# Kernel optimization log

Hardware: AMD Instinct MI355X
Metric: run time of the kernel (lower is better)

Reference implementation:

```python
import jax, jax.numpy as jnp
import numpy as np

K = 16  # kNN size (self included)
R = 4   # upsampling ratio


def _knn(pts, k):
    # pts: (B,N,3) -> idx (B,N,k); smallest distance first, so idx[:,:,0] is self
    sq = jnp.sum(pts * pts, axis=-1)
    d = sq[:, :, None] - 2.0 * jnp.einsum('bnd,bmd->bnm', pts, pts) + sq[:, None, :]
    _, idx = jax.lax.top_k(-d, k)
    return idx


def _gather(feats, idx):
    # feats (B,N,C), idx (B,N,k) -> (B,N,k,C)
    return jax.vmap(lambda f, i: f[i])(feats, idx)


def _conv1d(x, w, b):  # pointwise Conv1d: x (B,C,N)
    return jnp.einsum('oc,bcn->bon', w, x) + b[None, :, None]


def _conv2d(x, w, b):  # pointwise Conv2d: x (B,C,N,K)
    return jnp.einsum('oc,bcnk->bonk', w, x) + b[None, :, None, None]


def setup_inputs() -> dict:
    key = jax.random.key(0)
    ks = jax.random.split(key, 16)
    B, N = 2, 8192
    w = lambda k, s: jax.random.normal(k, s, jnp.float32) * 0.1
    return {
        'x': jax.random.normal(ks[0], (B, 3, N), jnp.float32),
        'mlp1_w1': w(ks[1], (32, 3)), 'mlp1_b1': jnp.zeros((32,), jnp.float32),
        'mlp1_w2': w(ks[2], (64, 32)), 'mlp1_b2': jnp.zeros((64,), jnp.float32),
        'mlp2_w1': w(ks[3], (32, 9)), 'mlp2_b1': jnp.zeros((32,), jnp.float32),
        'mlp3_w1': w(ks[4], (128, 96)), 'mlp3_b1': jnp.zeros((128,), jnp.float32),
        'mlp3_w2': w(ks[5], (12, 128)), 'mlp3_b2': jnp.zeros((12,), jnp.float32),
        'att_w1': w(ks[6], (128, 64)), 'att_b1': jnp.zeros((128,), jnp.float32),
        'att_w2': w(ks[7], (64, 128)), 'att_b2': jnp.zeros((64,), jnp.float32),
    }


def reference(x, mlp1_w1, mlp1_b1, mlp1_w2, mlp1_b2, mlp2_w1, mlp2_b1,
              mlp3_w1, mlp3_b1, mlp3_w2, mlp3_b2,
              att_w1, att_b1, att_w2, att_b2):
    B, C, N = x.shape
    pts = jnp.transpose(x, (0, 2, 1))                     # (B,N,3)
    idx = _knn(jax.lax.stop_gradient(pts), K)             # (B,N,K)

    # local 3x3 covariance features -> (B,9,N)
    nb = _gather(pts, idx)                                # (B,N,K,3)
    c = nb - jnp.mean(nb, axis=2, keepdims=True)
    cov = jnp.einsum('bnki,bnkj->bnij', c, c) / K         # (B,N,3,3)
    cov_feat = jnp.transpose(cov.reshape(B, N, 9), (0, 2, 1))

    # mlp1: 3 -> 32 -> 64, relu on both (last_act=True)
    f1 = jax.nn.relu(_conv1d(jax.nn.relu(_conv1d(x, mlp1_w1, mlp1_b1)), mlp1_w2, mlp1_b2))

    # gather neighbor features (exclude self) and form relative features
    fk = _gather(jnp.transpose(f1, (0, 2, 1)), idx[:, :, 1:])   # (B,N,K-1,64)
    f_knn = jnp.transpose(fk, (0, 3, 1, 2)) - f1[:, :, :, None]  # (B,64,N,K-1)

    # attention MLP (2D): 64 -> 128 -> 64, softmax over neighbor axis
    h = jax.nn.relu(_conv2d(f_knn, att_w1, att_b1))
    w = jax.nn.softmax(_conv2d(h, att_w2, att_b2), axis=-1)
    f_agg = jnp.sum(w * f_knn, axis=-1)                   # (B,64,N)

    # mlp2: 9 -> 32 with relu
    f_cov = jax.nn.relu(_conv1d(cov_feat, mlp2_w1, mlp2_b1))     # (B,32,N)

    f = jnp.concatenate([f_agg, f_cov], axis=1)           # (B,96,N)
    g = _conv1d(jax.nn.relu(_conv1d(f, mlp3_w1, mlp3_b1)), mlp3_w2, mlp3_b2)  # (B,3R,N)

    return jnp.tile(x, (1, 1, R)) + 0.15 * g.reshape(B, -1, R * N)
```

## Files before the change

kernel.cpp:

```cpp
#include <hip/hip_runtime.h>

#define BB 2
#define NN 8192
#define KK 16
#define QPB 64
#define PRE 256
#define STASH 32
#define EPSF 0.02f
typedef unsigned long long ull;
typedef unsigned short ushort;
#define KINF 0xFFFFFFFFFFFFFFFFULL
#define BFONE 0x3F80

typedef __attribute__((ext_vector_type(8))) short short8;
typedef __attribute__((ext_vector_type(4))) float f32x4;

static __device__ __forceinline__ ushort f2bf(float f) {
    unsigned u = __float_as_uint(f);
    unsigned r = (u + 0x7FFFu + ((u >> 16) & 1u)) >> 16;
    return (ushort)r;
}
static __device__ __forceinline__ float bf2f(ushort s) {
    return __uint_as_float(((unsigned)s) << 16);
}

static __device__ __forceinline__ float distq(const float4& qp, const float4& cn) {
    return fmaf(qp.x, cn.x, fmaf(qp.y, cn.y, fmaf(qp.z, cn.z, __fadd_rn(qp.w, cn.w))));
}

__global__ __launch_bounds__(256) void prep_f1_kernel(
    const float* __restrict__ x, float4* __restrict__ pts4, float4* __restrict__ pts4n,
    ushort* __restrict__ ptsC64,
    const float* __restrict__ w1, const float* __restrict__ b1,
    const float* __restrict__ w2, const float* __restrict__ b2,
    ushort* __restrict__ f1)
{
    if (blockIdx.x < 64) {
        int t = blockIdx.x * 256 + threadIdx.x;
        int b = t >> 13, n = t & (NN - 1);
        float x0 = x[(b * 3 + 0) * NN + n];
        float x1 = x[(b * 3 + 1) * NN + n];
        float x2 = x[(b * 3 + 2) * NN + n];
        float sq = fmaf(x2, x2, fmaf(x1, x1, __fmul_rn(x0, x0)));
        pts4[t]  = make_float4(x0, x1, x2, sq);
        pts4n[t] = make_float4(-2.f * x0, -2.f * x1, -2.f * x2, sq);

        float m2x = -2.f * x0, m2y = -2.f * x1, m2z = -2.f * x2;
        ushort hx = f2bf(m2x), hy = f2bf(m2y), hz = f2bf(m2z);
        ushort lx = f2bf(m2x - bf2f(hx));
        ushort ly = f2bf(m2y - bf2f(hy));
        ushort lz = f2bf(m2z - bf2f(hz));
        ushort sh = f2bf(sq), sl = f2bf(sq - bf2f(sh));
        short8 r0 = { (short)hx, (short)hy, (short)hz, (short)lx,
                      (short)ly, (short)lz, (short)hx, (short)hy };
        short8 r1 = { (short)hz, (short)lx, (short)ly, (short)lz,
                      (short)sh, (short)sl, (short)BFONE, (short)BFONE };
        short8 zz = { 0, 0, 0, 0, 0, 0, 0, 0 };
        ushort* cp = ptsC64 + (size_t)t * 32;
        *(short8*)(cp)      = r0;
        *(short8*)(cp + 8)  = r1;
        *(short8*)(cp + 16) = zz;
        *(short8*)(cp + 24) = zz;
    } else {
        int P = (blockIdx.x - 64) * 256 + threadIdx.x;
        int b = P >> 13, n = P & (NN - 1);
        float x0 = x[(b * 3 + 0) * NN + n];
        float x1 = x[(b * 3 + 1) * NN + n];
        float x2 = x[(b * 3 + 2) * NN + n];
        float h[32];
#pragma unroll
        for (int o = 0; o < 32; ++o) {
            float v = fmaf(w1[o * 3 + 2], x2, fmaf(w1[o * 3 + 1], x1, fmaf(w1[o * 3 + 0], x0, b1[o])));
            h[o] = fmaxf(v, 0.f);
        }
#pragma unroll
        for (int o4 = 0; o4 < 16; ++o4) {
            float vv[4];
#pragma unroll
            for (int u = 0; u < 4; ++u) {
                int o = o4 * 4 + u;
                float v = b2[o];
#pragma unroll
                for (int k = 0; k < 32; ++k) v = fmaf(w2[o * 32 + k], h[k], v);
                vv[u] = fmaxf(v, 0.f);
            }
            ushort4 s = { f2bf(vv[0]), f2bf(vv[1]), f2bf(vv[2]), f2bf(vv[3]) };
            *(ushort4*)(f1 + (size_t)P * 64 + o4 * 4) = s;
        }
    }
}

__global__ __launch_bounds__(512) void knn_prefix_kernel(
    const float4* __restrict__ pts4, const float4* __restrict__ pts4n,
    float* __restrict__ thrb)
{
    __shared__ float pbuf[11 * 512];
    __shared__ float smem[8 * 4 * 64];

    const int t    = threadIdx.x;
    const int wv   = t >> 6;
    const int lane = t & 63;
    const int b    = blockIdx.y;
    const int q    = blockIdx.x * QPB + lane;
    const int sl   = __builtin_amdgcn_readfirstlane(wv);

    const float4 qp = pts4[b * NN + q];
    const float4* __restrict__ cp = pts4n + (size_t)b * NN + (size_t)sl * 1024;

    float l0 = 3.0e38f, l1 = 3.0e38f, l2 = 3.0e38f, l3 = 3.0e38f;
    float curmax = 3.0e38f;
    int pend = 0;

    for (int i0 = 0; i0 < PRE; i0 += 8) {
#pragma unroll
        for (int u = 0; u < 8; ++u) {
            float d = distq(qp, cp[i0 + u]);
            pbuf[pend * 512 + t] = d;
            pend += (d < curmax) ? 1 : 0;
        }
        if (__any(pend >= 4)) {
            for (int j = 0; j < 11; ++j) {
                if (!__any(j < pend)) break;
                float v = pbuf[j * 512 + t];
                float k = (j < pend) ? v : 3.0e38f;
                bool b3 = k < l3, b2 = k < l2, b1 = k < l1, b0 = k < l0;
                l3 = b3 ? (b2 ? l2 : k) : l3;
                l2 = b2 ? (b1 ? l1 : k) : l2;
                l1 = b1 ? (b0 ? l0 : k) : l1;
                l0 = b0 ? k : l0;
            }
            pend = 0;
            curmax = l3;
        }
    }
    for (int j = 0; j < 11; ++j) {
        if (!__any(j < pend)) break;
        float v = pbuf[j * 512 + t];
        float k = (j < pend) ? v : 3.0e38f;
        bool b3 = k < l3, b2 = k < l2, b1 = k < l1, b0 = k < l0;
        l3 = b3 ? (b2 ? l2 : k) : l3;
        l2 = b2 ? (b1 ? l1 : k) : l2;
        l1 = b1 ? (b0 ? l0 : k) : l1;
        l0 = b0 ? k : l0;
    }

    __syncthreads();
    smem[(wv * 4 + 0) * 64 + lane] = l0;
    smem[(wv * 4 + 1) * 64 + lane] = l1;
    smem[(wv * 4 + 2) * 64 + lane] = l2;
    smem[(wv * 4 + 3) * 64 + lane] = l3;
    __syncthreads();

    if (t < QPB) {
        float h[8];
        int kc[8];
#pragma unroll
        for (int s = 0; s < 8; ++s) { h[s] = smem[(s * 4) * 64 + t]; kc[s] = 0; }
        float best = 3.0e38f;
        for (int o = 0; o < KK; ++o) {
            best = h[0]; int bs = 0;
#pragma unroll
            for (int s = 1; s < 8; ++s) { if (h[s] < best) { best = h[s]; bs = s; } }
#pragma unroll
            for (int s = 0; s < 8; ++s) {
                if (s == bs) {
                    kc[s]++;
                    h[s] = (kc[s] < 4) ? smem[(s * 4 + kc[s]) * 64 + t] : 3.0e38f;
                }
            }
        }
        thrb[(size_t)b * NN + blockIdx.x * QPB + t] = best;
    }
}

__global__ __launch_bounds__(256) void knn_scan_kernel(
    const float4* __restrict__ pts4, const ushort* __restrict__ ptsC64,
    const float* __restrict__ thrb, unsigned* __restrict__ bufm)
{
    __shared__ __align__(16) char lbuf[10240];

    const int t    = threadIdx.x;
    const int wv   = t >> 6;
    const int lane = t & 63;
    const int l15  = lane & 15, l4 = lane >> 4;
    const int b    = blockIdx.y;
    const int z    = blockIdx.z;
    const int qt   = blockIdx.x * 4 + wv;
    const int qbase = qt * 16;

    const float4 p = pts4[(size_t)b * NN + qbase + l15];
    const ushort qhx = f2bf(p.x), qhy = f2bf(p.y), qhz = f2bf(p.z);
    const ushort qlx = f2bf(p.x - bf2f(qhx));
    const ushort qly = f2bf(p.y - bf2f(qhy));
    const ushort qlz = f2bf(p.z - bf2f(qhz));
    const ushort qsh = f2bf(p.w), qsl = f2bf(p.w - bf2f(qsh));
    short8 qf;
    if (l4 == 0)
        qf = short8{ (short)qhx, (short)qhy, (short)qhz, (short)qhx,
                     (short)qhy, (short)qhz, (short)qlx, (short)qly };
    else if (l4 == 1)
        qf = short8{ (short)qlz, (short)qlx, (short)qly, (short)qlz,
                     (short)BFONE, (short)BFONE, (short)qsh, (short)qsl };
    else
        qf = short8{ 0, 0, 0, 0, 0, 0, 0, 0 };

    const float thrq = thrb[(size_t)b * NN + qbase + l15] * 1.001f + EPSF;

    const uint4* __restrict__ gsrc =
        (const uint4*)(ptsC64 + ((size_t)b * NN + (size_t)z * 1024) * 32);

    unsigned* __restrict__ op =
        bufm + (size_t)(b * NN + qbase + l15) * 256 + z * 32 + l4 * 8;

    uint4 r0 = gsrc[t], r1 = gsrc[t + 256];
    unsigned w4[4];

#pragma unroll 1
    for (int g = 0; g < 8; ++g) {
        __syncthreads();
        *(uint4*)(lbuf + (t >> 2) * 80 + (t & 3) * 16) = r0;
        *(uint4*)(lbuf + ((t + 256) >> 2) * 80 + (t & 3) * 16) = r1;
        if (g < 7) {
            r0 = gsrc[(g + 1) * 512 + t];
            r1 = gsrc[(g + 1) * 512 + t + 256];
        }
        __syncthreads();

        unsigned acc = 0;
#pragma unroll
        for (int i = 0; i < 8; ++i) {
            short8 cf = *(const short8*)(lbuf + (i * 16 + l15) * 80 + l4 * 16);
            f32x4 D = { 0.f, 0.f, 0.f, 0.f };
            D = __builtin_amdgcn_mfma_f32_16x16x32_bf16(cf, qf, D, 0, 0, 0);
            acc = acc * 2u + (unsigned)(D[0] <= thrq);
            acc = acc * 2u + (unsigned)(D[1] <= thrq);
            acc = acc * 2u + (unsigned)(D[2] <= thrq);
            acc = acc * 2u + (unsigned)(D[3] <= thrq);
        }
        w4[g & 3] = acc;
        if ((g & 3) == 3)
            *(uint4*)(op + (g >> 2) * 4) = make_uint4(w4[0], w4[1], w4[2], w4[3]);
    }
}

__global__ __launch_bounds__(256) void knn_select_kernel(
    const float4* __restrict__ pts4, const float4* __restrict__ pts4n,
    const unsigned* __restrict__ bufm,
    int* __restrict__ iout)
{
    __shared__ ull sm3[4][8][8][KK];
    __shared__ ushort stash[STASH][256];

    const int t = threadIdx.x;
    const int wv = t >> 6, lane = t & 63;
    const int qq = lane & 7, hh = lane >> 3;
    const int q  = (blockIdx.x * 4 + wv) * 8 + qq;
    const int b  = q >> 13;

    const float4 qp = pts4[q];
    ull list[KK];
#pragma unroll
    for (int i = 0; i < KK; ++i) list[i] = KINF;

    const unsigned* __restrict__ mrow = bufm + (size_t)q * 256 + hh * 32;
    int pend = 0;
#pragma unroll 1
    for (int g4 = 0; g4 < 8; ++g4) {
        uint4 v = ((const uint4*)mrow)[g4];
        unsigned wsv[4] = { v.x, v.y, v.z, v.w };
#pragma unroll
        for (int j = 0; j < 4; ++j) {
            unsigned w = wsv[j];
            const int W = hh * 32 + g4 * 4 + j;
            const int cb = ((W >> 5) << 10) + ((W & 7) << 7) + (((W >> 3) & 3) << 2);
            while (w) {
                int p = __builtin_ctz(w);
                w &= w - 1;
                int m = 31 - p;
                int id = cb + ((m >> 2) << 4) + (m & 3);
                if (pend < STASH) {
                    stash[pend][t] = (ushort)id;
                    ++pend;
                } else {
                    float d = distq(qp, pts4n[b * NN + id]);
                    unsigned ud = __float_as_uint(d);
                    ud ^= ((unsigned)((int)ud >> 31)) | 0x80000000u;
                    ull k = ((ull)ud << 32) | (unsigned)id;
#pragma unroll
                    for (int i2 = KK - 1; i2 > 0; --i2) {
                        bool c1 = k < list[i2];
                        bool c2 = k < list[i2 - 1];
                        ull nd = c2 ? list[i2 - 1] : k;
                        list[i2] = c1 ? nd : list[i2];
                    }
                    list[0] = (k < list[0]) ? k : list[0];
                }
            }
        }
    }

    for (int j = 0; ; j += 2) {
        if (!__any(j < pend)) break;
        int j1 = j + 1;
        int id0 = stash[(j  < pend) ? j  : 0][t];
        int id1 = stash[(j1 < pend) ? j1 : 0][t];
        float4 cn0 = pts4n[b * NN + id0];
        float4 cn1 = pts4n[b * NN + id1];

        float d0 = distq(qp, cn0);
        unsigned ud0 = __float_as_uint(d0);
        ud0 ^= ((unsigned)((int)ud0 >> 31)) | 0x80000000u;
        ull k0 = (j < pend) ? ((((ull)ud0) << 32) | (unsigned)id0) : KINF;
#pragma unroll
        for (int i2 = KK - 1; i2 > 0; --i2) {
            bool c1 = k0 < list[i2];
            bool c2 = k0 < list[i2 - 1];
            ull nd = c2 ? list[i2 - 1] : k0;
            list[i2] = c1 ? nd : list[i2];
        }
        list[0] = (k0 < list[0]) ? k0 : list[0];

        float d1 = distq(qp, cn1);
        unsigned ud1 = __float_as_uint(d1);
        ud1 ^= ((unsigned)((int)ud1 >> 31)) | 0x80000000u;
        ull k1 = (j1 < pend) ? ((((ull)ud1) << 32) | (unsigned)id1) : KINF;
#pragma unroll
        for (int i2 = KK - 1; i2 > 0; --i2) {
            bool c1 = k1 < list[i2];
            bool c2 = k1 < list[i2 - 1];
            ull nd = c2 ? list[i2 - 1] : k1;
            list[i2] = c1 ? nd : list[i2];
        }
        list[0] = (k1 < list[0]) ? k1 : list[0];
    }

#pragma unroll
    for (int k = 0; k < KK; ++k) sm3[wv][hh][qq][k] = list[k];

    if (hh == 0) {
        ull h[8]; int kc[8];
#pragma unroll
        for (int s = 0; s < 8; ++s) { h[s] = sm3[wv][s][qq][0]; kc[s] = 0; }
        int* op = iout + (size_t)q * KK;
        for (int o = 0; o < KK; ++o) {
            ull best = h[0]; int bs = 0;
#pragma unroll
            for (int s = 1; s < 8; ++s) { if (h[s] < best) { best = h[s]; bs = s; } }
            op[o] = (int)(unsigned)(best & 0xFFFFFFFFULL);
#pragma unroll
            for (int s = 0; s < 8; ++s) {
                if (s == bs) {
                    kc[s]++;
                    h[s] = (kc[s] < KK) ? sm3[wv][s][qq][kc[s]] : KINF;
                }
            }
        }
    }
}

__global__ __launch_bounds__(256, 2) void attn_cov_kernel(
    const ushort* __restrict__ f1, const int* __restrict__ idx,
    const float* __restrict__ aw1, const float* __restrict__ ab1,
    const float* __restrict__ aw2, const float* __restrict__ ab2,
    ushort* __restrict__ fagg,
    const float4* __restrict__ pts4,
    const float* __restrict__ cw, const float* __restrict__ cb,
    ushort* __restrict__ fcov)
{
    __shared__ __align__(16) ushort w1l[128][72];
    __shared__ __align__(16) ushort w2l[64][136];
    __shared__ __align__(16) ushort fkb[4][16][72];
    __shared__ __align__(16) ushort hb[4][16][136];

    const int t = threadIdx.x;

    if (blockIdx.x >= 512) {
        int P = (blockIdx.x - 512) * 256 + t;
        int b = P >> 13;
        const int4* ip4 = (const int4*)(idx + (size_t)P * KK);
        int ids[KK];
#pragma unroll
        for (int g = 0; g < 4; ++g) {
            int4 v = ip4[g];
            ids[g * 4 + 0] = v.x; ids[g * 4 + 1] = v.y;
            ids[g * 4 + 2] = v.z; ids[g * 4 + 3] = v.w;
        }
        float px[KK], py[KK], pz[KK];
#pragma unroll
        for (int k = 0; k < KK; ++k) {
            float4 c = pts4[b * NN + ids[k]];
            px[k] = c.x; py[k] = c.y; pz[k] = c.z;
        }
        float mx = 0.f, my = 0.f, mz = 0.f;
#pragma unroll
        for (int k = 0; k < KK; ++k) { mx += px[k]; my += py[k]; mz += pz[k]; }
        mx *= (1.f / 16.f); my *= (1.f / 16.f); mz *= (1.f / 16.f);
        float c00 = 0, c01 = 0, c02 = 0, c11 = 0, c12 = 0, c22 = 0;
#pragma unroll
        for (int k = 0; k < KK; ++k) {
            float dx = px[k] - mx, dy = py[k] - my, dz = pz[k] - mz;
            c00 = fmaf(dx, dx, c00); c01 = fmaf(dx, dy, c01); c02 = fmaf(dx, dz, c02);
            c11 = fmaf(dy, dy, c11); c12 = fmaf(dy, dz, c12); c22 = fmaf(dz, dz, c22);
        }
        const float inv = 1.f / 16.f;
        float cf[9] = { c00 * inv, c01 * inv, c02 * inv,
                        c01 * inv, c11 * inv, c12 * inv,
                        c02 * inv, c12 * inv, c22 * inv };
        ushort* outp = fcov + (size_t)P * 32;
#pragma unroll
        for (int o = 0; o < 32; ++o) {
            float v = cb[o];
#pragma unroll
            for (int m = 0; m < 9; ++m) v = fmaf(cw[o * 9 + m], cf[m], v);
            outp[o] = f2bf(fmaxf(v, 0.f));
        }
        return;
    }

    const int wv = t >> 6, lane = t & 63;
    const int l15 = lane & 15, qd = lane >> 4;

    for (int i = t; i < 128 * 64; i += 256) {
        int r = i >> 6, c = i & 63;
        w1l[r][c] = f2bf(aw1[i]);
    }
    for (int i = t; i < 64 * 128; i += 256) {
        int r = i >> 7, c = i & 127;
        w2l[r][c] = f2bf(aw2[i]);
    }
    __syncthreads();

    const int W = blockIdx.x * 4 + wv;
    for (int g = 0; g < 8; ++g) {
        const int P = W * 8 + g;
        const int b = P >> 13;

        float fc = bf2f(f1[(size_t)P * 64 + lane]);
        ushort fn[15];
#pragma unroll
        for (int j = 0; j < 15; ++j) {
            int nb = idx[(size_t)P * KK + 1 + j];
            fn[j] = f1[((size_t)b * NN + nb) * 64 + lane];
        }
#pragma unroll
        for (int j = 0; j < 15; ++j) fkb[wv][j][lane] = f2bf(bf2f(fn[j]) - fc);
        fkb[wv][15][lane] = 0;

        short8 a0 = *(const short8*)&fkb[wv][l15][qd * 8];
        short8 a1 = *(const short8*)&fkb[wv][l15][32 + qd * 8];

#pragma unroll
        for (int tile = 0; tile < 8; ++tile) {
            float bv = ab1[tile * 16 + l15];
            f32x4 acc = { bv, bv, bv, bv };
            short8 b0 = *(const short8*)&w1l[tile * 16 + l15][qd * 8];
            short8 b1f = *(const short8*)&w1l[tile * 16 + l15][32 + qd * 8];
            acc = __builtin_amdgcn_mfma_f32_16x16x32_bf16(a0, b0, acc, 0, 0, 0);
            acc = __builtin_amdgcn_mfma_f32_16x16x32_bf16(a1, b1f, acc, 0, 0, 0);
#pragma unroll
            for (int reg = 0; reg < 4; ++reg)
                hb[wv][qd * 4 + reg][tile * 16 + l15] = f2bf(fmaxf(acc[reg], 0.f));
        }

        short8 a2[4];
#pragma unroll
        for (int ks = 0; ks < 4; ++ks)
            a2[ks] = *(const short8*)&hb[wv][l15][ks * 32 + qd * 8];

        f32x4 L[4];
#pragma unroll
        for (int tile = 0; tile < 4; ++tile) {
            float bv = ab2[tile * 16 + l15];
            f32x4 acc = { bv, bv, bv, bv };
#pragma unroll
            for (int ks = 0; ks < 4; ++ks) {
                short8 bf = *(const short8*)&w2l[tile * 16 + l15][ks * 32 + qd * 8];
                acc = __builtin_amdgcn_mfma_f32_16x16x32_bf16(a2[ks], bf, acc, 0, 0, 0);
            }
            L[tile] = acc;
        }

        float fa[4];
#pragma unroll
        for (int tile = 0; tile < 4; ++tile) {
            float m1 = -3.0e38f;
#pragma unroll
            for (int reg = 0; reg < 4; ++reg)
                if (qd * 4 + reg < 15) m1 = fmaxf(m1, L[tile][reg]);
            m1 = fmaxf(m1, __shfl_xor(m1, 16));
            m1 = fmaxf(m1, __shfl_xor(m1, 32));
            float e[4], ssum = 0.f;
#pragma unroll
            for (int reg = 0; reg < 4; ++reg) {
                bool valid = (qd * 4 + reg < 15);
                e[reg] = valid ? __expf(L[tile][reg] - m1) : 0.f;
                ssum += e[reg];
            }
            ssum += __shfl_xor(ssum, 16);
            ssum += __shfl_xor(ssum, 32);
            float part = 0.f;
#pragma unroll
            for (int reg = 0; reg < 4; ++reg) {
                float fkv = bf2f(fkb[wv][qd * 4 + reg][tile * 16 + l15]);
                part = fmaf(e[reg], fkv, part);
            }
            part += __shfl_xor(part, 16);
            part += __shfl_xor(part, 32);
            fa[tile] = part / ssum;
        }
        if (qd == 0) {
#pragma unroll
            for (int tile = 0; tile < 4; ++tile)
                fagg[(size_t)P * 64 + tile * 16 + l15] = f2bf(fa[tile]);
        }
    }
}

__global__ __launch_bounds__(256) void mlp3_kernel(
    const ushort* __restrict__ fagg, const ushort* __restrict__ fcov,
    const float* __restrict__ w1, const float* __restrict__ b1,
    const float* __restrict__ w2, const float* __restrict__ b2,
    const float* __restrict__ x, float* __restrict__ out)
{
    __shared__ __align__(16) ushort fb[4][16][104];
    __shared__ __align__(16) ushort hb[4][16][136];

    const int t = threadIdx.x;
    const int wv = t >> 6, lane = t & 63;
    const int l15 = lane & 15, qd = lane >> 4;

    short8 w1f[8][3];
#pragma unroll
    for (int tile = 0; tile < 8; ++tile)
#pragma unroll
        for (int ks = 0; ks < 3; ++ks) {
            const float* p = w1 + ((size_t)(tile * 16 + l15) * 96 + ks * 32 + qd * 8);
            float4 A = *(const float4*)p, B = *(const float4*)(p + 4);
            short8 f;
            f[0] = f2bf(A.x); f[1] = f2bf(A.y); f[2] = f2bf(A.z); f[3] = f2bf(A.w);
            f[4] = f2bf(B.x); f[5] = f2bf(B.y); f[6] = f2bf(B.z); f[7] = f2bf(B.w);
            w1f[tile][ks] = f;
        }
    short8 w2f[4];
#pragma unroll
    for (int ks = 0; ks < 4; ++ks) {
        short8 f = {};
        if (l15 < 12) {
            const float* p = w2 + ((size_t)l15 * 128 + ks * 32 + qd * 8);
            float4 A = *(const float4*)p, B = *(const float4*)(p + 4);
            f[0] = f2bf(A.x); f[1] = f2bf(A.y); f[2] = f2bf(A.z); f[3] = f2bf(A.w);
            f[4] = f2bf(B.x); f[5] = f2bf(B.y); f[6] = f2bf(B.z); f[7] = f2bf(B.w);
        }
        w2f[ks] = f;
    }

    const int T = blockIdx.x * 4 + wv;

    {
        const int pt = lane >> 2, c4 = lane & 3;
        const ushort* fap = fagg + ((size_t)(T * 16 + pt) * 64 + c4 * 16);
        *(short8*)&fb[wv][pt][c4 * 16]     = *(const short8*)(fap);
        *(short8*)&fb[wv][pt][c4 * 16 + 8] = *(const short8*)(fap + 8);
        const ushort* fcp = fcov + ((size_t)(T * 16 + pt) * 32 + c4 * 8);
        *(short8*)&fb[wv][pt][64 + c4 * 8] = *(const short8*)(fcp);
    }

    short8 a[3];
#pragma unroll
    for (int ks = 0; ks < 3; ++ks)
        a[ks] = *(const short8*)&fb[wv][l15][ks * 32 + qd * 8];

#pragma unroll
    for (int tile = 0; tile < 8; ++tile) {
        float bv = b1[tile * 16 + l15];
        f32x4 acc = { bv, bv, bv, bv };
#pragma unroll
        for (int ks = 0; ks < 3; ++ks)
            acc = __builtin_amdgcn_mfma_f32_16x16x32_bf16(a[ks], w1f[tile][ks], acc, 0, 0, 0);
#pragma unroll
        for (int reg = 0; reg < 4; ++reg)
            hb[wv][qd * 4 + reg][tile * 16 + l15] = f2bf(fmaxf(acc[reg], 0.f));
    }

    short8 a2[4];
#pragma unroll
    for (int ks = 0; ks < 4; ++ks)
        a2[ks] = *(const short8*)&hb[wv][l15][ks * 32 + qd * 8];

    float bv2 = (l15 < 12) ? b2[l15] : 0.f;
    f32x4 acc = { bv2, bv2, bv2, bv2 };
#pragma unroll
    for (int ks = 0; ks < 4; ++ks)
        acc = __builtin_amdgcn_mfma_f32_16x16x32_bf16(a2[ks], w2f[ks], acc, 0, 0, 0);

    if (l15 < 12) {
        const int c = l15 >> 2, rr = l15 & 3;
#pragma unroll
        for (int reg = 0; reg < 4; ++reg) {
            int P = T * 16 + qd * 4 + reg;
            int b = P >> 13, n = P & (NN - 1);
            float xv = x[((size_t)b * 3 + c) * NN + n];
            out[(((size_t)b * 3 + c) * 4 + rr) * NN + n] = xv + 0.15f * acc[reg];
        }
    }
}

extern "C" void kernel_launch(void* const* d_in, const int* in_sizes, int n_in,
                              void* d_out, int out_size, void* d_ws, size_t ws_size,
                              hipStream_t stream)
{
    (void)in_sizes; (void)n_in; (void)out_size; (void)ws_size;
    const float* x    = (const float*)d_in[0];
    const float* m1w1 = (const float*)d_in[1];
    const float* m1b1 = (const float*)d_in[2];
    const float* m1w2 = (const float*)d_in[3];
    const float* m1b2 = (const float*)d_in[4];
    const float* m2w1 = (const float*)d_in[5];
    const float* m2b1 = (const float*)d_in[6];
    const float* m3w1 = (const float*)d_in[7];
    const float* m3b1 = (const float*)d_in[8];
    const float* m3w2 = (const float*)d_in[9];
    const float* m3b2 = (const float*)d_in[10];
    const float* aw1  = (const float*)d_in[11];
    const float* ab1  = (const float*)d_in[12];
    const float* aw2  = (const float*)d_in[13];
    const float* ab2  = (const float*)d_in[14];
    float* out = (float*)d_out;

    char* ws = (char*)d_ws;
    float4* pts4   = (float4*)(ws + 0);
    float4* pts4n  = (float4*)(ws + 262144);
    float*  thrb   = (float*)(ws + 524288);
    int*    idxb   = (int*)  (ws + 589824);
    ushort* ptsC64 = (ushort*)(ws + 1638400);
    unsigned* bufm = (unsigned*)(ws + 2686976);
    ushort* f1b    = (ushort*)(ws + 19464192);
    ushort* fagg   = (ushort*)(ws + 21561344);
    ushort* fcov   = (ushort*)(ws + 23658496);

    prep_f1_kernel<<<128, 256, 0, stream>>>(x, pts4, pts4n, ptsC64, m1w1, m1b1, m1w2, m1b2, f1b);
    knn_prefix_kernel<<<dim3(NN / QPB, BB), 512, 0, stream>>>(pts4, pts4n, thrb);
    knn_scan_kernel<<<dim3(128, BB, 8), 256, 0, stream>>>(pts4, ptsC64, thrb, bufm);
    knn_select_kernel<<<512, 256, 0, stream>>>(pts4, pts4n, bufm, idxb);
    attn_cov_kernel<<<576, 256, 0, stream>>>(f1b, idxb, aw1, ab1, aw2, ab2, fagg,
                                             pts4, m2w1, m2b1, fcov);
    mlp3_kernel<<<256, 256, 0, stream>>>(fagg, fcov, m3w1, m3b1, m3w2, m3b2, x, out);
}
```

Measured before the change: 253.7 us.

## Split kNN prefix threshold across 16 waves with double-buffered candidate loads

The prefix kernel that estimates a per-query kNN distance threshold now runs 1024 threads (16 waves) instead of 512. Each wave scans a 128-point prefix of a 512-point slice, down from 256 points of a 1024-point slice. Candidate loads are double-buffered in registers so the next 8 points are fetched while the current 8 are processed. The final merge covers 16 per-wave top-4 lists instead of 8. Total prefix samples stay at 2048 per query, but the threshold may differ, which can change how many candidates the later scan keeps. The larger block also uses more shared memory.

```diff
diff --git a/kernel.cpp b/kernel.cpp
--- a/kernel.cpp
+++ b/kernel.cpp
@@ -4,7 +4,8 @@
 #define NN 8192
 #define KK 16
 #define QPB 64
-#define PRE 256
+#define PRE2 128
+#define SLICE 512
 #define STASH 32
 #define EPSF 0.02f
 typedef unsigned long long ull;
@@ -90,12 +91,26 @@
     }
 }
 
-__global__ __launch_bounds__(512) void knn_prefix_kernel(
+#define DRAIN_TOP4()                                             \
+    {                                                            \
+        for (int j = 0; j < 11; ++j) {                           \
+            if (!__any(j < pend)) break;                         \
+            float v = pbuf[j * 1024 + t];                        \
+            float k = (j < pend) ? v : 3.0e38f;                  \
+            bool b3 = k < l3, b2 = k < l2, b1 = k < l1, b0 = k < l0; \
+            l3 = b3 ? (b2 ? l2 : k) : l3;                        \
+            l2 = b2 ? (b1 ? l1 : k) : l2;                        \
+            l1 = b1 ? (b0 ? l0 : k) : l1;                        \
+            l0 = b0 ? k : l0;                                    \
+        }                                                        \
+    }
+
+__global__ __launch_bounds__(1024, 4) void knn_prefix_kernel(
     const float4* __restrict__ pts4, const float4* __restrict__ pts4n,
     float* __restrict__ thrb)
 {
-    __shared__ float pbuf[11 * 512];
-    __shared__ float smem[8 * 4 * 64];
+    __shared__ float pbuf[11 * 1024];
+    __shared__ float smem[16 * 4 * 64];
 
     const int t    = threadIdx.x;
     const int wv   = t >> 6;
@@ -105,44 +120,40 @@
     const int sl   = __builtin_amdgcn_readfirstlane(wv);
 
     const float4 qp = pts4[b * NN + q];
-    const float4* __restrict__ cp = pts4n + (size_t)b * NN + (size_t)sl * 1024;
+    const float4* __restrict__ cp = pts4n + (size_t)b * NN + (size_t)sl * SLICE;
 
     float l0 = 3.0e38f, l1 = 3.0e38f, l2 = 3.0e38f, l3 = 3.0e38f;
     float curmax = 3.0e38f;
     int pend = 0;
 
-    for (int i0 = 0; i0 < PRE; i0 += 8) {
+    float4 ca[8], cb2[8];
+#pragma unroll
+    for (int u = 0; u < 8; ++u) ca[u] = cp[u];
+
+#pragma unroll 1
+    for (int i0 = 0; i0 < PRE2; i0 += 16) {
+#pragma unroll
+        for (int u = 0; u < 8; ++u) cb2[u] = cp[i0 + 8 + u];
 #pragma unroll
         for (int u = 0; u < 8; ++u) {
-            float d = distq(qp, cp[i0 + u]);
-            pbuf[pend * 512 + t] = d;
+            float d = distq(qp, ca[u]);
+            pbuf[pend * 1024 + t] = d;
             pend += (d < curmax) ? 1 : 0;
         }
-        if (__any(pend >= 4)) {
-            for (int j = 0; j < 11; ++j) {
-                if (!__any(j < pend)) break;
-                float v = pbuf[j * 512 + t];
-                float k = (j < pend) ? v : 3.0e38f;
-                bool b3 = k < l3, b2 = k < l2, b1 = k < l1, b0 = k < l0;
-                l3 = b3 ? (b2 ? l2 : k) : l3;
-                l2 = b2 ? (b1 ? l1 : k) : l2;
-                l1 = b1 ? (b0 ? l0 : k) : l1;
-                l0 = b0 ? k : l0;
-            }
-            pend = 0;
-            curmax = l3;
-        }
-    }
-    for (int j = 0; j < 11; ++j) {
-        if (!__any(j < pend)) break;
-        float v = pbuf[j * 512 + t];
-        float k = (j < pend) ? v : 3.0e38f;
-        bool b3 = k < l3, b2 = k < l2, b1 = k < l1, b0 = k < l0;
-        l3 = b3 ? (b2 ? l2 : k) : l3;
-        l2 = b2 ? (b1 ? l1 : k) : l2;
-        l1 = b1 ? (b0 ? l0 : k) : l1;
-        l0 = b0 ? k : l0;
-    }
+        if (__any(pend >= 4)) { DRAIN_TOP4(); pend = 0; curmax = l3; }
+        if (i0 + 16 < PRE2) {
+#pragma unroll
+            for (int u = 0; u < 8; ++u) ca[u] = cp[i0 + 16 + u];
+        }
+#pragma unroll
+        for (int u = 0; u < 8; ++u) {
+            float d = distq(qp, cb2[u]);
+            pbuf[pend * 1024 + t] = d;
+            pend += (d < curmax) ? 1 : 0;
+        }
+        if (__any(pend >= 4)) { DRAIN_TOP4(); pend = 0; curmax = l3; }
+    }
+    DRAIN_TOP4();
 
     __syncthreads();
     smem[(wv * 4 + 0) * 64 + lane] = l0;
@@ -152,17 +163,17 @@
     __syncthreads();
 
     if (t < QPB) {
-        float h[8];
-        int kc[8];
-#pragma unroll
-        for (int s = 0; s < 8; ++s) { h[s] = smem[(s * 4) * 64 + t]; kc[s] = 0; }
+        float h[16];
+        int kc[16];
+#pragma unroll
+        for (int s = 0; s < 16; ++s) { h[s] = smem[(s * 4) * 64 + t]; kc[s] = 0; }
         float best = 3.0e38f;
         for (int o = 0; o < KK; ++o) {
             best = h[0]; int bs = 0;
 #pragma unroll
-            for (int s = 1; s < 8; ++s) { if (h[s] < best) { best = h[s]; bs = s; } }
-#pragma unroll
-            for (int s = 0; s < 8; ++s) {
+            for (int s = 1; s < 16; ++s) { if (h[s] < best) { best = h[s]; bs = s; } }
+#pragma unroll
+            for (int s = 0; s < 16; ++s) {
                 if (s == bs) {
                     kc[s]++;
                     h[s] = (kc[s] < 4) ? smem[(s * 4 + kc[s]) * 64 + t] : 3.0e38f;
@@ -639,7 +650,7 @@
     ushort* fcov   = (ushort*)(ws + 23658496);
 
     prep_f1_kernel<<<128, 256, 0, stream>>>(x, pts4, pts4n, ptsC64, m1w1, m1b1, m1w2, m1b2, f1b);
-    knn_prefix_kernel<<<dim3(NN / QPB, BB), 512, 0, stream>>>(pts4, pts4n, thrb);
+    knn_prefix_kernel<<<dim3(NN / QPB, BB), 1024, 0, stream>>>(pts4, pts4n, thrb);
     knn_scan_kernel<<<dim3(128, BB, 8), 256, 0, stream>>>(pts4, ptsC64, thrb, bufm);
     knn_select_kernel<<<512, 256, 0, stream>>>(pts4, pts4n, bufm, idxb);
     attn_cov_kernel<<<576, 256, 0, stream>>>(f1b, idxb, aw1, ab1, aw2, ab2, fagg,
```

Result: faster. 239.7 us (-5.5%).
